# Kernel optimization log

Hardware: AMD Instinct MI355X
Metric: run time of the kernel (lower is better)

The kernel has to match this reference:

```python
import jax, jax.numpy as jnp
import numpy as np
import math

EMBED_DIM = 1024
NUM_HEADS = 16
HEAD_DIM = EMBED_DIM // NUM_HEADS
B, S = 2, 2048


def setup_inputs() -> dict:
    key = jax.random.key(0)
    ks = jax.random.split(key, 13)
    sc = 1.0 / math.sqrt(EMBED_DIM)
    inp = {
        "query": jax.random.normal(ks[0], (B, S, EMBED_DIM), jnp.float32),
        "key": jax.random.normal(ks[1], (B, S, EMBED_DIM), jnp.float32),
        "value": jax.random.normal(ks[2], (B, S, EMBED_DIM), jnp.float32),
        "input_patch_mask": jax.random.randint(ks[3], (B, S), 0, 2, jnp.int32),
        "Wq": jax.random.normal(ks[4], (EMBED_DIM, EMBED_DIM), jnp.float32) * sc,
        "bq": jnp.zeros((EMBED_DIM,), jnp.float32),
        "Wk": jax.random.normal(ks[5], (EMBED_DIM, EMBED_DIM), jnp.float32) * sc,
        "bk": jnp.zeros((EMBED_DIM,), jnp.float32),
        "Wv": jax.random.normal(ks[6], (EMBED_DIM, EMBED_DIM), jnp.float32) * sc,
        "bv": jnp.zeros((EMBED_DIM,), jnp.float32),
        "Wo": jax.random.normal(ks[7], (EMBED_DIM, EMBED_DIM), jnp.float32) * sc,
        "bo": jnp.zeros((EMBED_DIM,), jnp.float32),
    }
    return inp


def _masked_softmax(scores, mask):
    # Equivalent to masked_fill(-inf) -> softmax -> nan_to_num(0.0):
    # fully-masked rows produce exactly 0, without generating NaNs.
    neg_inf = jnp.array(-jnp.inf, scores.dtype)
    s = jnp.where(mask, scores, neg_inf)
    m = jnp.max(s, axis=-1, keepdims=True)
    m_safe = jnp.where(jnp.isfinite(m), m, jnp.zeros_like(m))
    e = jnp.where(mask, jnp.exp(s - m_safe), 0.0)
    denom = jnp.sum(e, axis=-1, keepdims=True)
    denom = jnp.where(denom == 0.0, 1.0, denom)
    return e / denom


def reference(query, key, value, input_patch_mask, Wq, bq, Wk, bk, Wv, bv, Wo, bo):
    b, s, d = query.shape
    h, hd = NUM_HEADS, HEAD_DIM
    q = (query @ Wq.T + bq).reshape(b, s, h, hd).transpose(0, 2, 1, 3)  # [b,h,s,hd]
    k = (key @ Wk.T + bk).reshape(b, s, h, hd).transpose(0, 2, 1, 3)
    v = (value @ Wv.T + bv).reshape(b, s, h, hd).transpose(0, 2, 1, 3)
    scores = jnp.einsum("bhqd,bhkd->bhqk", q, k) / math.sqrt(hd)
    # mask[b,i,j] = patch_mask[b,i] * patch_mask[b,j]
    mask = (input_patch_mask[:, :, None] * input_patch_mask[:, None, :]) > 0
    attn = _masked_softmax(scores, mask[:, None, :, :])  # dropout in eval mode = identity
    context = jnp.einsum("bhqk,bhkd->bhqd", attn, v)
    context = context.transpose(0, 2, 1, 3).reshape(b, s, d)
    return context @ Wo.T + bo
```

## Files before the change

kernel.cpp:

```cpp
#include <hip/hip_runtime.h>
#include <cstdint>
#include <cstddef>

#define EMBED 1024
#define NHEAD 16
#define HD    64
#define BATCH 2
#define SEQ   2048
#define MROWS (BATCH*SEQ)
#define QSCALE 0.1803368801111137f

typedef __bf16 bf16;
typedef __bf16 bf16x8 __attribute__((ext_vector_type(8)));
typedef float  f32x4  __attribute__((ext_vector_type(4)));
typedef unsigned int u32;

#if __has_builtin(__builtin_amdgcn_exp2f)
#define EXP2(x) __builtin_amdgcn_exp2f(x)
#else
#define EXP2(x) exp2f(x)
#endif

typedef const u32 __attribute__((address_space(1)))* gp_t;
typedef u32 __attribute__((address_space(3)))* lp_t;

__device__ __forceinline__ void g2l16(const void* g, void* l) {
  __builtin_amdgcn_global_load_lds((gp_t)(uintptr_t)g, (lp_t)(u32)(uintptr_t)l, 16, 0, 0);
}

#define MFMA(a, b, c) __builtin_amdgcn_mfma_f32_16x16x32_bf16((a), (b), (c), 0, 0, 0)

#define SZX8 ((MROWS*EMBED)/8)
#define SZW8 ((EMBED*EMBED)/8)

__global__ void cast_all(const float* __restrict__ q, const float* __restrict__ k,
                         const float* __restrict__ v, const float* __restrict__ wq,
                         const float* __restrict__ wk, const float* __restrict__ wv,
                         const float* __restrict__ wo,
                         bf16* xq, bf16* xk, bf16* xv,
                         bf16* wqb, bf16* wkb, bf16* wvb, bf16* wob) {
  int z = blockIdx.y;
  const float* in; bf16* out;
  switch (z) {
    case 0: in = q;  out = xq;  break;
    case 1: in = k;  out = xk;  break;
    case 2: in = v;  out = xv;  break;
    case 3: in = wq; out = wqb; break;
    case 4: in = wk; out = wkb; break;
    case 5: in = wv; out = wvb; break;
    default: in = wo; out = wob; break;
  }
  int n8 = (z < 3) ? SZX8 : SZW8;
  int i = blockIdx.x * blockDim.x + threadIdx.x;
  if (i >= n8) return;
  const float4* p = (const float4*)in;
  float4 a = p[2*i], b = p[2*i+1];
  union { bf16 h[8]; uint4 u; } r;
  r.h[0] = (bf16)a.x; r.h[1] = (bf16)a.y; r.h[2] = (bf16)a.z; r.h[3] = (bf16)a.w;
  r.h[4] = (bf16)b.x; r.h[5] = (bf16)b.y; r.h[6] = (bf16)b.z; r.h[7] = (bf16)b.w;
  ((uint4*)out)[i] = r.u;
}

#define BM 128
#define BN 128
#define BK 32
#define NKI (EMBED/BK)

__device__ __forceinline__ void gemm_core(
    const bf16* __restrict__ A, const bf16* __restrict__ W,
    int m0, int n0, bf16* Al, bf16* Bl, f32x4 (&acc)[4][4])
{
  const int tid  = threadIdx.x;
  const int lane = tid & 63, wid = tid >> 6;
  const int quad = lane >> 4, l16 = lane & 15;
  const int wm = wid >> 1, wn = wid & 1;

  const int R = tid >> 2, Cc = tid & 3;
  const int gcol = (Cc ^ ((R >> 1) & 3)) * 8;
  const bf16* Ag = A + (size_t)(m0 + R) * EMBED + gcol;
  const bf16* Bg = W + (size_t)(n0 + R) * EMBED + gcol;
  bf16* AlW = Al + wid * 512;
  bf16* BlW = Bl + wid * 512;

#define GSTAGE(ki) do { \
    const int nb_ = (ki) % 3; const int k0_ = (ki) * BK; \
    g2l16(Ag + k0_,                    AlW + nb_*4096); \
    g2l16(Ag + (size_t)64*EMBED + k0_, AlW + nb_*4096 + 2048); \
    g2l16(Bg + k0_,                    BlW + nb_*4096); \
    g2l16(Bg + (size_t)64*EMBED + k0_, BlW + nb_*4096 + 2048); } while (0)

  GSTAGE(0);
  GSTAGE(1);

  for (int ki = 0; ki < NKI; ++ki) {
    if (ki < NKI - 1) asm volatile("s_waitcnt vmcnt(4)" ::: "memory");
    else              asm volatile("s_waitcnt vmcnt(0)" ::: "memory");
    __builtin_amdgcn_s_barrier();
    __builtin_amdgcn_sched_barrier(0);
    if (ki + 2 < NKI) GSTAGE(ki + 2);

    const bf16* Ac = Al + (ki % 3)*4096;
    const bf16* Bc = Bl + (ki % 3)*4096;
    bf16x8 af[4], bg[4];
#pragma unroll
    for (int i = 0; i < 4; ++i) {
      int ra = wm*64 + i*16 + l16;
      af[i] = *(const bf16x8*)(Ac + ra*32 + ((quad ^ ((ra>>1)&3))*8));
      int rb = wn*64 + i*16 + l16;
      bg[i] = *(const bf16x8*)(Bc + rb*32 + ((quad ^ ((rb>>1)&3))*8));
    }
#pragma unroll
    for (int i = 0; i < 4; ++i)
#pragma unroll
      for (int j = 0; j < 4; ++j)
        acc[i][j] = MFMA(af[i], bg[j], acc[i][j]);
  }
#undef GSTAGE
}

__global__ __launch_bounds__(256) void qkv_kernel(
    const bf16* __restrict__ Xq, const bf16* __restrict__ Xk, const bf16* __restrict__ Xv,
    const bf16* __restrict__ Wq, const bf16* __restrict__ Wk, const bf16* __restrict__ Wv,
    const float* __restrict__ bq, const float* __restrict__ bk, const float* __restrict__ bv,
    bf16* __restrict__ Qp, bf16* __restrict__ Kp, bf16* __restrict__ VTg)
{
  __shared__ bf16 Al[3*BM*BK];
  __shared__ bf16 Bl[3*BN*BK];

  const unsigned hw = blockIdx.x + 8u*blockIdx.y + 256u*blockIdx.z;
  const unsigned wk = (hw & 7u)*96u + (hw >> 3);
  const int z  = (int)(wk >> 8);
  const unsigned rem = wk & 255u;
  const int by = (int)(rem >> 3), bx = (int)(rem & 7u);

  const bf16* A = z==0 ? Xq : z==1 ? Xk : Wv;
  const bf16* W = z==0 ? Wq : z==1 ? Wk : Xv;
  const float* bias = z==0 ? bq : z==1 ? bk : bv;
  const float scale = (z==0) ? QSCALE : 1.0f;
  const int m0 = (z < 2) ? by * BM : bx * BM;
  const int n0 = (z < 2) ? bx * BN : by * BN;

  f32x4 acc[4][4] = {};
  gemm_core(A, W, m0, n0, Al, Bl, acc);

  const int lane = threadIdx.x & 63, wid = threadIdx.x >> 6;
  const int quad = lane >> 4, l16 = lane & 15;
  const int wm = wid >> 1, wn = wid & 1;

  if (z < 2) {
#pragma unroll
    for (int i = 0; i < 4; ++i) {
#pragma unroll
      for (int j = 0; j < 4; ++j) {
        int col = n0 + wn*64 + j*16 + l16;
        float bv2 = bias[col];
        bf16* outp = (z == 0) ? Qp : Kp;
#pragma unroll
        for (int r = 0; r < 4; ++r) {
          int row = m0 + wm*64 + i*16 + quad*4 + r;
          outp[(size_t)row*EMBED + col] = (bf16)((acc[i][j][r] + bv2) * scale);
        }
      }
    }
  } else {
    const int tcol0 = n0 + wn*64;
    const int bb   = tcol0 >> 11;
    const int tile = (tcol0 & (SEQ-1)) >> 6;
    const int pbase = (l16 >> 2)*8 + (l16 & 3)*2;
#pragma unroll
    for (int i = 0; i < 4; ++i) {
      float4 bv4 = *(const float4*)&bias[m0 + wm*64 + i*16 + quad*4];
#pragma unroll
      for (int r = 0; r < 4; ++r) {
        int e = m0 + wm*64 + i*16 + quad*4 + r;
        int hh = e >> 6, dd = e & (HD-1);
        float bvr = (r==0) ? bv4.x : (r==1) ? bv4.y : (r==2) ? bv4.z : bv4.w;
        union { bf16 h[2]; u32 u; } p01, p23;
        p01.h[0] = (bf16)(acc[i][0][r] + bvr);
        p01.h[1] = (bf16)(acc[i][1][r] + bvr);
        p23.h[0] = (bf16)(acc[i][2][r] + bvr);
        p23.h[1] = (bf16)(acc[i][3][r] + bvr);
        size_t base = (((size_t)bb*NHEAD + hh)*HD + dd)*SEQ + tile*64;
        *(u32*)&VTg[base + pbase]      = p01.u;
        *(u32*)&VTg[base + 32 + pbase] = p23.u;
      }
    }
  }
}

__global__ __launch_bounds__(256) void oproj_kernel(
    const bf16* __restrict__ Ctx, const bf16* __restrict__ Wo,
    const float* __restrict__ bo, float* __restrict__ out)
{
  __shared__ bf16 Al[3*128*32];
  __shared__ bf16 Bl[3*64*32];
  const int tid  = threadIdx.x;
  const int lane = tid & 63, wid = tid >> 6;
  const int quad = lane >> 4, l16 = lane & 15;

  const unsigned hw = blockIdx.x + 16u*blockIdx.y;
  const unsigned wk = (hw & 7u)*64u + (hw >> 3);
  const int m0 = (int)(wk >> 4) * 128, n0 = (int)(wk & 15u) * 64;

  const int R = tid >> 2, Cc = tid & 3;
  const int gcol = (Cc ^ ((R >> 1) & 3)) * 8;
  const bf16* Ag = Ctx + (size_t)(m0 + R) * EMBED + gcol;
  const bf16* Bg = Wo  + (size_t)(n0 + R) * EMBED + gcol;
  bf16* AlW = Al + wid * 512;
  bf16* BlW = Bl + wid * 512;

#define OSTAGE(ki) do { \
    const int nb_ = (ki) % 3; const int k0_ = (ki) * BK; \
    g2l16(Ag + k0_,                    AlW + nb_*4096); \
    g2l16(Ag + (size_t)64*EMBED + k0_, AlW + nb_*4096 + 2048); \
    g2l16(Bg + k0_,                    BlW + nb_*2048); } while (0)

  OSTAGE(0);
  OSTAGE(1);

  f32x4 acc[2][4] = {};
  for (int ki = 0; ki < NKI; ++ki) {
    if (ki < NKI - 1) asm volatile("s_waitcnt vmcnt(3)" ::: "memory");
    else              asm volatile("s_waitcnt vmcnt(0)" ::: "memory");
    __builtin_amdgcn_s_barrier();
    __builtin_amdgcn_sched_barrier(0);
    if (ki + 2 < NKI) OSTAGE(ki + 2);

    const bf16* Ac = Al + (ki % 3)*4096;
    const bf16* Bc = Bl + (ki % 3)*2048;
    bf16x8 af[2], bg[4];
#pragma unroll
    for (int u = 0; u < 2; ++u) {
      int ra = wid*32 + u*16 + l16;
      af[u] = *(const bf16x8*)(Ac + ra*32 + ((quad ^ ((ra>>1)&3))*8));
    }
#pragma unroll
    for (int j = 0; j < 4; ++j) {
      int rb = j*16 + l16;
      bg[j] = *(const bf16x8*)(Bc + rb*32 + ((quad ^ ((rb>>1)&3))*8));
    }
#pragma unroll
    for (int u = 0; u < 2; ++u)
#pragma unroll
      for (int j = 0; j < 4; ++j)
        acc[u][j] = MFMA(af[u], bg[j], acc[u][j]);
  }
#undef OSTAGE

#pragma unroll
  for (int u = 0; u < 2; ++u)
#pragma unroll
    for (int j = 0; j < 4; ++j) {
      int col = n0 + j*16 + l16;
      float bv = bo[col];
#pragma unroll
      for (int r = 0; r < 4; ++r) {
        int row = m0 + wid*32 + u*16 + quad*4 + r;
        out[(size_t)row*EMBED + col] = (acc[u][j][r] + bv);
      }
    }
}

#define NT  (SEQ/64)

__global__ __launch_bounds__(512, 2) void attn_kernel(
    const bf16* __restrict__ Qp, const bf16* __restrict__ Kp, const bf16* __restrict__ VT,
    const int* __restrict__ pmask, bf16* __restrict__ Ctx)
{
  __shared__ __align__(16) bf16 SM[5*4096];

  const unsigned hw = blockIdx.x + 16u*blockIdx.y + 256u*blockIdx.z;
  const unsigned wkb = (hw & 7u)*64u + (hw >> 3);
  const int qt = (int)(wkb & 15u);
  const unsigned pair = wkb >> 4;
  const int h = (int)(pair & 15u), b = (int)(pair >> 4);

  const int tid = threadIdx.x, lane = tid & 63, wid = tid >> 6;
  const int quad = lane >> 4, l16 = lane & 15;
  const int w4 = wid & 3, h2 = wid >> 2;
  const int qrow0 = qt*128 + w4*32;

  bf16x8 qf[2][2];
#pragma unroll
  for (int qg = 0; qg < 2; ++qg) {
    const size_t qoff = (size_t)(b*SEQ + qrow0 + qg*16 + l16)*EMBED + h*HD;
    qf[qg][0] = *(const bf16x8*)(Qp + qoff + quad*8);
    qf[qg][1] = *(const bf16x8*)(Qp + qoff + 32 + quad*8);
  }

  bf16 onev = (bf16)1.0f;
  bf16x8 ones = {onev, onev, onev, onev, onev, onev, onev, onev};

  const bf16* Kg  = Kp + (size_t)b*SEQ*EMBED + h*HD;
  const bf16* VTg = VT + (size_t)(b*NHEAD + h)*HD*SEQ;
  const int*  kmw = pmask + b*SEQ + h2*32 + quad*4;

  const int R = tid >> 3;
  const int Cc = tid & 7;
  const int scol = (Cc ^ (R & 7)) * 8;

  f32x4 o[2][4] = {};
  f32x4 lacc[2] = {};
  bf16x8 pa[2] = {};

#define STAGE_K(kt, buf) g2l16(Kg + (size_t)((kt)*64 + R)*EMBED + scol, SM + (buf)*4096 + wid*512)
#define STAGE_V(kt, buf) g2l16(VTg + (size_t)R*SEQ + (kt)*64 + scol,    SM + 8192 + (buf)*4096 + wid*512)

  int4 kq0 = *(const int4*)(kmw);
  int4 kq1 = *(const int4*)(kmw + 16);
  STAGE_K(0, 0);
  STAGE_V(0, 0);

  for (int kt = 0; kt < NT; ++kt) {
    asm volatile("s_waitcnt vmcnt(0)" ::: "memory");
    __builtin_amdgcn_s_barrier();
    __builtin_amdgcn_sched_barrier(0);

    float fm0[4], fm1[4];
    fm0[0] = (float)kq0.x; fm0[1] = (float)kq0.y; fm0[2] = (float)kq0.z; fm0[3] = (float)kq0.w;
    fm1[0] = (float)kq1.x; fm1[1] = (float)kq1.y; fm1[2] = (float)kq1.z; fm1[3] = (float)kq1.w;
    __builtin_amdgcn_sched_barrier(0);

    if (kt + 1 < NT) {
      kq0 = *(const int4*)(kmw + (kt+1)*64);
      kq1 = *(const int4*)(kmw + (kt+1)*64 + 16);
      STAGE_K(kt + 1, (kt + 1) & 1);
      STAGE_V(kt + 1, (kt + 1) % 3);
    }

    if (kt > 0) {
      const bf16* Vc = SM + 8192 + ((kt - 1) % 3)*4096;
      lacc[0] = MFMA(pa[0], ones, lacc[0]);
      lacc[1] = MFMA(pa[1], ones, lacc[1]);
#pragma unroll
      for (int t = 0; t < 4; ++t) {
        int rd = t*16 + l16, sd = rd & 7;
        bf16x8 vf = *(const bf16x8*)(Vc + rd*64 + (((h2*4 + quad) ^ sd)*8));
        o[0][t] = MFMA(pa[0], vf, o[0][t]);
        o[1][t] = MFMA(pa[1], vf, o[1][t]);
      }
    }

    const bf16* Kc = SM + (kt & 1)*4096;
#pragma unroll
    for (int kg = 0; kg < 2; ++kg) {
      int ra = h2*32 + kg*16 + l16, sa = ra & 7;
      bf16x8 kfa = *(const bf16x8*)(Kc + ra*64 + ((quad       ^ sa)*8));
      bf16x8 kfb = *(const bf16x8*)(Kc + ra*64 + (((quad + 4) ^ sa)*8));
      const float* fm = kg ? fm1 : fm0;
#pragma unroll
      for (int qg = 0; qg < 2; ++qg) {
        f32x4 s = {};
        s = MFMA(kfa, qf[qg][0], s);
        s = MFMA(kfb, qf[qg][1], s);
        pa[qg][0 + kg] = (bf16)(EXP2(s[0]) * fm[0]);
        pa[qg][2 + kg] = (bf16)(EXP2(s[1]) * fm[1]);
        pa[qg][4 + kg] = (bf16)(EXP2(s[2]) * fm[2]);
        pa[qg][6 + kg] = (bf16)(EXP2(s[3]) * fm[3]);
      }
    }
  }

  {
    const bf16* Vc = SM + 8192 + ((NT - 1) % 3)*4096;
    lacc[0] = MFMA(pa[0], ones, lacc[0]);
    lacc[1] = MFMA(pa[1], ones, lacc[1]);
#pragma unroll
    for (int t = 0; t < 4; ++t) {
      int rd = t*16 + l16, sd = rd & 7;
      bf16x8 vf = *(const bf16x8*)(Vc + rd*64 + (((h2*4 + quad) ^ sd)*8));
      o[0][t] = MFMA(pa[0], vf, o[0][t]);
      o[1][t] = MFMA(pa[1], vf, o[1][t]);
    }
  }

  __syncthreads();
  f32x4* rp = (f32x4*)SM;
  const int idx = w4*64 + lane;
  if (h2 == 1) {
#pragma unroll
    for (int qg = 0; qg < 2; ++qg) {
#pragma unroll
      for (int t = 0; t < 4; ++t) rp[(qg*4 + t)*256 + idx] = o[qg][t];
      rp[2048 + qg*256 + idx] = lacc[qg];
    }
  }
  __syncthreads();
  if (h2 == 0) {
#pragma unroll
    for (int qg = 0; qg < 2; ++qg) {
      lacc[qg] += rp[2048 + qg*256 + idx];
#pragma unroll
      for (int t = 0; t < 4; ++t) o[qg][t] += rp[(qg*4 + t)*256 + idx];
    }
#pragma unroll
    for (int qg = 0; qg < 2; ++qg) {
      int4 qm = *(const int4*)(pmask + b*SEQ + qrow0 + qg*16 + quad*4);
      float inv[4];
      inv[0] = (qm.x && lacc[qg][0] > 0.f) ? 1.0f / lacc[qg][0] : 0.0f;
      inv[1] = (qm.y && lacc[qg][1] > 0.f) ? 1.0f / lacc[qg][1] : 0.0f;
      inv[2] = (qm.z && lacc[qg][2] > 0.f) ? 1.0f / lacc[qg][2] : 0.0f;
      inv[3] = (qm.w && lacc[qg][3] > 0.f) ? 1.0f / lacc[qg][3] : 0.0f;
#pragma unroll
      for (int t = 0; t < 4; ++t)
#pragma unroll
        for (int r = 0; r < 4; ++r) {
          int row = b*SEQ + qrow0 + qg*16 + quad*4 + r;
          Ctx[(size_t)row*EMBED + h*HD + t*16 + l16] = (bf16)(o[qg][t][r] * inv[r]);
        }
    }
  }
}

extern "C" void kernel_launch(void* const* d_in, const int* in_sizes, int n_in,
                              void* d_out, int out_size, void* d_ws, size_t ws_size,
                              hipStream_t stream)
{
  const float* query = (const float*)d_in[0];
  const float* key   = (const float*)d_in[1];
  const float* value = (const float*)d_in[2];
  const int*   pm    = (const int*)d_in[3];
  const float* Wq = (const float*)d_in[4];
  const float* bq = (const float*)d_in[5];
  const float* Wk = (const float*)d_in[6];
  const float* bk = (const float*)d_in[7];
  const float* Wv = (const float*)d_in[8];
  const float* bv = (const float*)d_in[9];
  const float* Wo = (const float*)d_in[10];
  const float* bo = (const float*)d_in[11];
  float* out = (float*)d_out;

  const size_t SZ_X = (size_t)MROWS * EMBED;
  const size_t SZ_W = (size_t)EMBED * EMBED;

  bf16* p   = (bf16*)d_ws;
  bf16* Xq  = p; p += SZ_X;
  bf16* Xk  = p; p += SZ_X;
  bf16* Xv  = p; p += SZ_X;
  bf16* Wqb = p; p += SZ_W;
  bf16* Wkb = p; p += SZ_W;
  bf16* Wvb = p; p += SZ_W;
  bf16* Wob = p; p += SZ_W;
  bf16* Qp  = p; p += SZ_X;
  bf16* Kp  = p; p += SZ_X;
  bf16* VTg = p; p += SZ_X;
  bf16* Ctx = p; p += SZ_X;

  dim3 gc((unsigned)(SZX8/256), 7);
  cast_all<<<gc, 256, 0, stream>>>(query, key, value, Wq, Wk, Wv, Wo,
                                   Xq, Xk, Xv, Wqb, Wkb, Wvb, Wob);

  dim3 gq(EMBED/BN, MROWS/BM, 3);
  qkv_kernel<<<gq, 256, 0, stream>>>(Xq, Xk, Xv, Wqb, Wkb, Wvb, bq, bk, bv, Qp, Kp, VTg);

  dim3 ga(SEQ/128, NHEAD, BATCH);
  attn_kernel<<<ga, 512, 0, stream>>>(Qp, Kp, VTg, pm, Ctx);

  dim3 gg(EMBED/64, MROWS/128);
  oproj_kernel<<<gg, 256, 0, stream>>>(Ctx, Wob, bo, out);
}
```

Measured before the change: 213.0 us.

## Double attention KV tile to 128 keys per iteration

The attention kernel now processes 128 keys per loop iteration instead of 64. K and V tiles are staged as two 64-row slabs, and each wave-half handles 64 keys with four score groups and two P slabs. This halves the number of barriers and loop iterations and packs more MFMA work between synchronisations. In exchange, LDS use doubles to 80 KB per block and register pressure rises. The launch-bounds occupancy hint is raised to 4 blocks, which that LDS footprint likely cannot meet.

New measurement: 219.3 us. 1.03x slower.

```diff
diff --git a/kernel.cpp b/kernel.cpp
--- a/kernel.cpp
+++ b/kernel.cpp
@@ -261,13 +261,14 @@
     }
 }
 
-#define NT  (SEQ/64)
-
-__global__ __launch_bounds__(512, 2) void attn_kernel(
+#define KVB 128
+#define NT  (SEQ/KVB)
+
+__global__ __launch_bounds__(512, 4) void attn_kernel(
     const bf16* __restrict__ Qp, const bf16* __restrict__ Kp, const bf16* __restrict__ VT,
     const int* __restrict__ pmask, bf16* __restrict__ Ctx)
 {
-  __shared__ __align__(16) bf16 SM[5*4096];
+  __shared__ __align__(16) bf16 SM[10*4096];
 
   const unsigned hw = blockIdx.x + 16u*blockIdx.y + 256u*blockIdx.z;
   const unsigned wkb = (hw & 7u)*64u + (hw >> 3);
@@ -293,7 +294,7 @@
 
   const bf16* Kg  = Kp + (size_t)b*SEQ*EMBED + h*HD;
   const bf16* VTg = VT + (size_t)(b*NHEAD + h)*HD*SEQ;
-  const int*  kmw = pmask + b*SEQ + h2*32 + quad*4;
+  const int*  kmw = pmask + b*SEQ + h2*64 + quad*4;
 
   const int R = tid >> 3;
   const int Cc = tid & 7;
@@ -301,13 +302,21 @@
 
   f32x4 o[2][4] = {};
   f32x4 lacc[2] = {};
-  bf16x8 pa[2] = {};
-
-#define STAGE_K(kt, buf) g2l16(Kg + (size_t)((kt)*64 + R)*EMBED + scol, SM + (buf)*4096 + wid*512)
-#define STAGE_V(kt, buf) g2l16(VTg + (size_t)R*SEQ + (kt)*64 + scol,    SM + 8192 + (buf)*4096 + wid*512)
+  bf16x8 pa[2][2] = {};
+
+#define KBUF(i) (SM + (i)*8192)
+#define VBUF(i) (SM + 16384 + (i)*8192)
+#define STAGE_K(kt, buf) do { \
+    g2l16(Kg + (size_t)((kt)*KVB + R)*EMBED + scol,      KBUF(buf) + wid*512); \
+    g2l16(Kg + (size_t)((kt)*KVB + R + 64)*EMBED + scol, KBUF(buf) + 4096 + wid*512); } while (0)
+#define STAGE_V(kt, buf) do { \
+    g2l16(VTg + (size_t)R*SEQ + (kt)*KVB + scol,      VBUF(buf) + wid*512); \
+    g2l16(VTg + (size_t)R*SEQ + (kt)*KVB + 64 + scol, VBUF(buf) + 4096 + wid*512); } while (0)
 
   int4 kq0 = *(const int4*)(kmw);
   int4 kq1 = *(const int4*)(kmw + 16);
+  int4 kq2 = *(const int4*)(kmw + 32);
+  int4 kq3 = *(const int4*)(kmw + 48);
   STAGE_K(0, 0);
   STAGE_V(0, 0);
 
@@ -316,61 +325,76 @@
     __builtin_amdgcn_s_barrier();
     __builtin_amdgcn_sched_barrier(0);
 
-    float fm0[4], fm1[4];
-    fm0[0] = (float)kq0.x; fm0[1] = (float)kq0.y; fm0[2] = (float)kq0.z; fm0[3] = (float)kq0.w;
-    fm1[0] = (float)kq1.x; fm1[1] = (float)kq1.y; fm1[2] = (float)kq1.z; fm1[3] = (float)kq1.w;
+    float fa[4], fb[4], fc2[4], fd[4];
+    fa[0]=(float)kq0.x;  fa[1]=(float)kq0.y;  fa[2]=(float)kq0.z;  fa[3]=(float)kq0.w;
+    fb[0]=(float)kq1.x;  fb[1]=(float)kq1.y;  fb[2]=(float)kq1.z;  fb[3]=(float)kq1.w;
+    fc2[0]=(float)kq2.x; fc2[1]=(float)kq2.y; fc2[2]=(float)kq2.z; fc2[3]=(float)kq2.w;
+    fd[0]=(float)kq3.x;  fd[1]=(float)kq3.y;  fd[2]=(float)kq3.z;  fd[3]=(float)kq3.w;
     __builtin_amdgcn_sched_barrier(0);
 
     if (kt + 1 < NT) {
-      kq0 = *(const int4*)(kmw + (kt+1)*64);
-      kq1 = *(const int4*)(kmw + (kt+1)*64 + 16);
+      kq0 = *(const int4*)(kmw + (kt+1)*KVB);
+      kq1 = *(const int4*)(kmw + (kt+1)*KVB + 16);
+      kq2 = *(const int4*)(kmw + (kt+1)*KVB + 32);
+      kq3 = *(const int4*)(kmw + (kt+1)*KVB + 48);
       STAGE_K(kt + 1, (kt + 1) & 1);
       STAGE_V(kt + 1, (kt + 1) % 3);
     }
 
     if (kt > 0) {
-      const bf16* Vc = SM + 8192 + ((kt - 1) % 3)*4096;
-      lacc[0] = MFMA(pa[0], ones, lacc[0]);
-      lacc[1] = MFMA(pa[1], ones, lacc[1]);
+      const bf16* Vc = VBUF((kt - 1) % 3) + h2*4096;
+      lacc[0] = MFMA(pa[0][0], ones, lacc[0]);
+      lacc[0] = MFMA(pa[0][1], ones, lacc[0]);
+      lacc[1] = MFMA(pa[1][0], ones, lacc[1]);
+      lacc[1] = MFMA(pa[1][1], ones, lacc[1]);
 #pragma unroll
       for (int t = 0; t < 4; ++t) {
         int rd = t*16 + l16, sd = rd & 7;
-        bf16x8 vf = *(const bf16x8*)(Vc + rd*64 + (((h2*4 + quad) ^ sd)*8));
-        o[0][t] = MFMA(pa[0], vf, o[0][t]);
-        o[1][t] = MFMA(pa[1], vf, o[1][t]);
+        bf16x8 vf0 = *(const bf16x8*)(Vc + rd*64 + ((quad       ^ sd)*8));
+        bf16x8 vf1 = *(const bf16x8*)(Vc + rd*64 + (((quad + 4) ^ sd)*8));
+        o[0][t] = MFMA(pa[0][0], vf0, o[0][t]);
+        o[0][t] = MFMA(pa[0][1], vf1, o[0][t]);
+        o[1][t] = MFMA(pa[1][0], vf0, o[1][t]);
+        o[1][t] = MFMA(pa[1][1], vf1, o[1][t]);
       }
     }
 
-    const bf16* Kc = SM + (kt & 1)*4096;
-#pragma unroll
-    for (int kg = 0; kg < 2; ++kg) {
-      int ra = h2*32 + kg*16 + l16, sa = ra & 7;
+    const bf16* Kc = KBUF(kt & 1);
+#pragma unroll
+    for (int kg = 0; kg < 4; ++kg) {
+      int ra = h2*64 + kg*16 + l16, sa = ra & 7;
       bf16x8 kfa = *(const bf16x8*)(Kc + ra*64 + ((quad       ^ sa)*8));
       bf16x8 kfb = *(const bf16x8*)(Kc + ra*64 + (((quad + 4) ^ sa)*8));
-      const float* fm = kg ? fm1 : fm0;
+      const float* fm = (kg==0) ? fa : (kg==1) ? fb : (kg==2) ? fc2 : fd;
+      const int slab = kg >> 1, kgl = kg & 1;
 #pragma unroll
       for (int qg = 0; qg < 2; ++qg) {
         f32x4 s = {};
         s = MFMA(kfa, qf[qg][0], s);
         s = MFMA(kfb, qf[qg][1], s);
-        pa[qg][0 + kg] = (bf16)(EXP2(s[0]) * fm[0]);
-        pa[qg][2 + kg] = (bf16)(EXP2(s[1]) * fm[1]);
-        pa[qg][4 + kg] = (bf16)(EXP2(s[2]) * fm[2]);
-        pa[qg][6 + kg] = (bf16)(EXP2(s[3]) * fm[3]);
+        pa[qg][slab][0 + kgl] = (bf16)(EXP2(s[0]) * fm[0]);
+        pa[qg][slab][2 + kgl] = (bf16)(EXP2(s[1]) * fm[1]);
+        pa[qg][slab][4 + kgl] = (bf16)(EXP2(s[2]) * fm[2]);
+        pa[qg][slab][6 + kgl] = (bf16)(EXP2(s[3]) * fm[3]);
       }
     }
   }
 
   {
-    const bf16* Vc = SM + 8192 + ((NT - 1) % 3)*4096;
-    lacc[0] = MFMA(pa[0], ones, lacc[0]);
-    lacc[1] = MFMA(pa[1], ones, lacc[1]);
+    const bf16* Vc = VBUF((NT - 1) % 3) + h2*4096;
+    lacc[0] = MFMA(pa[0][0], ones, lacc[0]);
+    lacc[0] = MFMA(pa[0][1], ones, lacc[0]);
+    lacc[1] = MFMA(pa[1][0], ones, lacc[1]);
+    lacc[1] = MFMA(pa[1][1], ones, lacc[1]);
 #pragma unroll
     for (int t = 0; t < 4; ++t) {
       int rd = t*16 + l16, sd = rd & 7;
-      bf16x8 vf = *(const bf16x8*)(Vc + rd*64 + (((h2*4 + quad) ^ sd)*8));
-      o[0][t] = MFMA(pa[0], vf, o[0][t]);
-      o[1][t] = MFMA(pa[1], vf, o[1][t]);
+      bf16x8 vf0 = *(const bf16x8*)(Vc + rd*64 + ((quad       ^ sd)*8));
+      bf16x8 vf1 = *(const bf16x8*)(Vc + rd*64 + (((quad + 4) ^ sd)*8));
+      o[0][t] = MFMA(pa[0][0], vf0, o[0][t]);
+      o[0][t] = MFMA(pa[0][1], vf1, o[0][t]);
+      o[1][t] = MFMA(pa[1][0], vf0, o[1][t]);
+      o[1][t] = MFMA(pa[1][1], vf1, o[1][t]);
     }
   }
 
```
